# Performance work log

Hardware: AMD Instinct MI355X
Metric: run time of the kernel (lower is better)

Reference implementation:

```python
import jax, jax.numpy as jnp
import numpy as np

REFSIZE = 1024  # init kwarg refsize -> self.N
EPS = float(np.finfo(np.float32).eps)


def interp1d(x, y, xnew):
    """Batched linear interpolation, faithful to Interp1d.forward.
    x, y: (D, N) with x sorted along last dim; xnew: (D, P). Returns (D, P)."""
    # torch.searchsorted default (right=False) == numpy/jnp side='left'
    ind = jax.vmap(jnp.searchsorted)(x, xnew) - 1
    ind = jnp.clip(ind, 0, x.shape[1] - 2)
    slopes = (y[:, 1:] - y[:, :-1]) / (EPS + (x[:, 1:] - x[:, :-1]))
    x_sel = jnp.take_along_axis(x, ind, axis=1)
    y_sel = jnp.take_along_axis(y, ind, axis=1)
    s_sel = jnp.take_along_axis(slopes, ind, axis=1)
    return y_sel + s_sel * (xnew - x_sel)


def setup_inputs() -> dict:
    key = jax.random.key(0)
    k1, k2 = jax.random.split(key)
    l, n = 2048, 4096
    x1 = jax.random.uniform(k1, (l, n), dtype=jnp.float32)  # points on [0,1)
    w = jax.random.uniform(k2, (l, n), dtype=jnp.float32)
    x1_weights = w / jnp.sum(w, axis=-1, keepdims=True)  # row-normalized masses
    return {"x1": x1, "x1_weights": x1_weights}


def reference(x1, x1_weights):
    l, n = x1.shape
    N = REFSIZE
    ref = jnp.linspace(0.0, 1.0, N + 1, dtype=jnp.float32)[:-1]  # (N,)

    # empirical_cdf: sort samples, cumsum weights
    order = jnp.argsort(x1, axis=-1)
    xs = jnp.take_along_axis(x1, order, axis=-1)          # (l, n) sorted samples
    ys = jnp.cumsum(jnp.take_along_axis(x1_weights, order, axis=-1), axis=-1)  # CDF

    # emb
    alpha = (jnp.sum(x1 * x1_weights, axis=-1) / jnp.sum(x1_weights, axis=-1) - 0.5)[:, None]
    xnew = jnp.broadcast_to(jnp.linspace(-1.0, 2.0, 3 * N, dtype=jnp.float32)[None, :], (l, 3 * N))
    int_x = jnp.floor(xnew)
    rest_x = xnew - int_x
    ecdf = int_x + interp1d(xs, ys, rest_x)               # (l, 3N) extended CDF

    x_grid = jnp.broadcast_to(ref[None, :], (l, N))
    embedd = interp1d(ecdf, xnew, x_grid - alpha) - x_grid  # inverse-CDF embedding

    # circular cost
    a = jnp.abs(embedd)
    m = jnp.minimum(a, 1.0 - a)
    return jnp.sqrt(jnp.mean(jnp.sum(m * m, axis=-1)) + 1e-8)
```

## Files before the change

### kernel.cpp

```cpp
#include <hip/hip_runtime.h>
#include <math.h>

#define L    2048
#define NCOL 4096
#define NG   1024
#define N3   3072
#define T    256
#define EPT  16
#define NB   2048
#define BPT  (NB / T)
#define FEPS 1.1920929e-07f

typedef unsigned long long u64;

__device__ __forceinline__ int lower_bound_f(const float* a, int lo, int hi, float v) {
  while (lo < hi) {
    int mid = (lo + hi) >> 1;
    if (a[mid] < v) lo = mid + 1; else hi = mid;
  }
  return lo;
}

__device__ __forceinline__ int bucket_of(u64 k) {
  float f = __uint_as_float((unsigned)(k >> 32));
  int b = (int)(f * (float)NB);
  return b > NB - 1 ? NB - 1 : b;
}

__global__ __launch_bounds__(T, 3) void lcot_rows(const float* __restrict__ X,
                                                  const float* __restrict__ W,
                                                  float* __restrict__ rowsum) {
  extern __shared__ char smem[];
  u64*   pairs = (u64*)smem;
  float* xs    = (float*)smem;
  float* ys    = xs + NCOL;
  int*   cnt   = (int*)(smem + 32768);
  float* ecdf  = (float*)(smem + 32768 + 8200);

  __shared__ float redA[4], redB[4], fwt[4];
  __shared__ int   iwt[4];
  __shared__ float s_alpha;

  const int tid  = threadIdx.x;
  const int lane = tid & 63;
  const int wave = tid >> 6;
  const int row  = blockIdx.x;
  const float* xr = X + (size_t)row * NCOL;
  const float* wr = W + (size_t)row * NCOL;

#pragma unroll
  for (int i = 0; i < BPT; ++i) cnt[tid + i * T] = 0;

  u64 key[EPT]; float wv[EPT];
  float sxw = 0.f, sw = 0.f;
  const float4* xr4 = (const float4*)xr;
  const float4* wr4 = (const float4*)wr;
#pragma unroll
  for (int c = 0; c < 4; ++c) {
    float4 xv = xr4[tid * 4 + c];
    float4 ww = wr4[tid * 4 + c];
    sxw += xv.x * ww.x + xv.y * ww.y + xv.z * ww.z + xv.w * ww.w;
    sw  += ww.x + ww.y + ww.z + ww.w;
    int b = 16 * tid + 4 * c;
    key[4*c+0] = ((u64)__float_as_uint(xv.x) << 32) | (unsigned)(b + 0);
    key[4*c+1] = ((u64)__float_as_uint(xv.y) << 32) | (unsigned)(b + 1);
    key[4*c+2] = ((u64)__float_as_uint(xv.z) << 32) | (unsigned)(b + 2);
    key[4*c+3] = ((u64)__float_as_uint(xv.w) << 32) | (unsigned)(b + 3);
    wv[4*c+0] = ww.x; wv[4*c+1] = ww.y; wv[4*c+2] = ww.z; wv[4*c+3] = ww.w;
  }
#pragma unroll
  for (int off = 32; off > 0; off >>= 1) {
    sxw += __shfl_down(sxw, off);
    sw  += __shfl_down(sw, off);
  }
  if (lane == 0) { redA[wave] = sxw; redB[wave] = sw; }
  __syncthreads();

  int ord[EPT];
#pragma unroll
  for (int e = 0; e < EPT; ++e) ord[e] = atomicAdd(&cnt[bucket_of(key[e])], 1);
  __syncthreads();
  if (tid == 0)
    s_alpha = (redA[0] + redA[1] + redA[2] + redA[3]) /
              (redB[0] + redB[1] + redB[2] + redB[3]) - 0.5f;

  int c8[BPT];
  int runi = 0;
#pragma unroll
  for (int j = 0; j < BPT; ++j) { c8[j] = cnt[tid * BPT + j]; runi += c8[j]; }
  int toti = runi, prei = runi;
#pragma unroll
  for (int off = 1; off < 64; off <<= 1) {
    int v = __shfl_up(prei, off);
    if (lane >= off) prei += v;
  }
  if (lane == 63) iwt[wave] = prei;
  __syncthreads();
  int wpre = 0;
#pragma unroll
  for (int w2 = 0; w2 < 4; ++w2) wpre += (w2 < wave) ? iwt[w2] : 0;
  int acc = wpre + prei - toti;
#pragma unroll
  for (int j = 0; j < BPT; ++j) { int t2 = acc; acc += c8[j]; cnt[tid * BPT + j] = t2; }
  if (tid == T - 1) cnt[NB] = acc;
  __syncthreads();

#pragma unroll
  for (int e = 0; e < EPT; ++e) pairs[cnt[bucket_of(key[e])] + ord[e]] = key[e];
  __syncthreads();

  int p[EPT];
#pragma unroll
  for (int e = 0; e < EPT; ++e) {
    int b = bucket_of(key[e]);
    int lo = cnt[b], m = cnt[b + 1] - lo;
    int r = 0;
    for (int q = 0; q < m; ++q) r += (pairs[lo + q] < key[e]) ? 1 : 0;
    p[e] = lo + r;
  }
  __syncthreads();

#pragma unroll
  for (int e = 0; e < EPT; ++e) {
    xs[p[e]] = __uint_as_float((unsigned)(key[e] >> 32));
    ys[p[e]] = wv[e];
  }
  __syncthreads();

  float lw[EPT];
  {
    const float4* y4 = (const float4*)(ys + 16 * tid);
    float4 a0 = y4[0], a1 = y4[1], a2 = y4[2], a3 = y4[3];
    lw[0]=a0.x; lw[1]=a0.y; lw[2]=a0.z; lw[3]=a0.w;
    lw[4]=a1.x; lw[5]=a1.y; lw[6]=a1.z; lw[7]=a1.w;
    lw[8]=a2.x; lw[9]=a2.y; lw[10]=a2.z; lw[11]=a2.w;
    lw[12]=a3.x; lw[13]=a3.y; lw[14]=a3.z; lw[15]=a3.w;
  }
  float runf = 0.f;
#pragma unroll
  for (int c = 0; c < EPT; ++c) { runf += lw[c]; lw[c] = runf; }
  float totf = runf, pref = runf;
#pragma unroll
  for (int off = 1; off < 64; off <<= 1) {
    float v = __shfl_up(pref, off);
    if (lane >= off) pref += v;
  }
  if (lane == 63) fwt[wave] = pref;
  __syncthreads();
  float wpf = 0.f;
#pragma unroll
  for (int w2 = 0; w2 < 4; ++w2) wpf += (w2 < wave) ? fwt[w2] : 0.f;
  float basef = wpf + pref - totf;
  {
    float4* y4 = (float4*)(ys + 16 * tid);
    y4[0] = make_float4(basef+lw[0],  basef+lw[1],  basef+lw[2],  basef+lw[3]);
    y4[1] = make_float4(basef+lw[4],  basef+lw[5],  basef+lw[6],  basef+lw[7]);
    y4[2] = make_float4(basef+lw[8],  basef+lw[9],  basef+lw[10], basef+lw[11]);
    y4[3] = make_float4(basef+lw[12], basef+lw[13], basef+lw[14], basef+lw[15]);
  }
  __syncthreads();

#pragma unroll
  for (int s = 0; s < N3 / T; ++s) {
    int j = tid + s * T;
    float xnew = -1.0f + (3.0f * (float)j) / 3071.0f;
    float ix = floorf(xnew);
    float rest = xnew - ix;
    int k = (int)(rest * (float)NB);
    k = k > NB - 1 ? NB - 1 : k;
    int lo = lower_bound_f(xs, cnt[k], cnt[k + 1], rest);
    int ind = lo - 1;
    ind = ind < 0 ? 0 : (ind > NCOL - 2 ? NCOL - 2 : ind);
    float x0 = xs[ind], x1v = xs[ind + 1];
    float y0 = ys[ind], y1v = ys[ind + 1];
    float slope = (y1v - y0) / (FEPS + (x1v - x0));
    ecdf[j] = ix + (y0 + slope * (rest - x0));
  }
  __syncthreads();

  float alpha = s_alpha;
  float accf = 0.f;
#pragma unroll
  for (int s = 0; s < NG / T; ++s) {
    int kq = tid + s * T;
    float xg = (float)kq / 1024.0f;
    float q = xg - alpha;
    int lo = lower_bound_f(ecdf, 0, N3, q);
    int ind = lo - 1;
    ind = ind < 0 ? 0 : (ind > N3 - 2 ? N3 - 2 : ind);
    float e0 = ecdf[ind], e1 = ecdf[ind + 1];
    float y0 = -1.0f + (3.0f * (float)ind) / 3071.0f;
    float y1 = -1.0f + (3.0f * (float)(ind + 1)) / 3071.0f;
    float slope = (y1 - y0) / (FEPS + (e1 - e0));
    float emb = y0 + slope * (q - e0) - xg;
    float a = fabsf(emb);
    float m = fminf(a, 1.0f - a);
    accf += m * m;
  }
#pragma unroll
  for (int off = 32; off > 0; off >>= 1) accf += __shfl_down(accf, off);
  if (lane == 0) redA[wave] = accf;
  __syncthreads();
  if (tid == 0) rowsum[row] = redA[0] + redA[1] + redA[2] + redA[3];
}

__global__ __launch_bounds__(256) void lcot_final(const float* __restrict__ rowsum,
                                                  float* __restrict__ out) {
  __shared__ float red[4];
  int t = threadIdx.x;
  float s = 0.f;
  for (int i = t; i < L; i += 256) s += rowsum[i];
#pragma unroll
  for (int off = 32; off > 0; off >>= 1) s += __shfl_down(s, off);
  if ((t & 63) == 0) red[t >> 6] = s;
  __syncthreads();
  if (t == 0) {
    float tot = red[0] + red[1] + red[2] + red[3];
    out[0] = sqrtf(tot / (float)L + 1e-8f);
  }
}

extern "C" void kernel_launch(void* const* d_in, const int* in_sizes, int n_in,
                              void* d_out, int out_size, void* d_ws, size_t ws_size,
                              hipStream_t stream) {
  const float* X = (const float*)d_in[0];
  const float* W = (const float*)d_in[1];
  float* rowsum = (float*)d_ws;
  size_t shbytes = 32768 + 8200 + (size_t)N3 * 4;
  hipLaunchKernelGGL(lcot_rows, dim3(L), dim3(T), shbytes, stream, X, W, rowsum);
  hipLaunchKernelGGL(lcot_final, dim3(1), dim3(256), 0, stream,
                     (const float*)rowsum, (float*)d_out);
}
```

Baseline: 194.5 us.

## Double threads per row and add bucket LUT for inverse-CDF search

Raises the per-row block from 256 to 512 threads with 8 elements per thread, adjusting the scans and reductions for 8 waves. It also builds a 257-entry lookup table over the extended CDF so each inverse-CDF query binary-searches a narrow window instead of all 3072 entries. The aim is more latency hiding per row and fewer LDS probes in the second search. The cost is more LDS per block and an extra barrier. The windowed search assumes the CDF maps each bucket to a small index range.

```diff
diff --git a/kernel.cpp b/kernel.cpp
--- a/kernel.cpp
+++ b/kernel.cpp
@@ -5,8 +5,9 @@
 #define NCOL 4096
 #define NG   1024
 #define N3   3072
-#define T    256
-#define EPT  16
+#define T    512
+#define NW   8
+#define EPT  8
 #define NB   2048
 #define BPT  (NB / T)
 #define FEPS 1.1920929e-07f
@@ -27,7 +28,7 @@
   return b > NB - 1 ? NB - 1 : b;
 }
 
-__global__ __launch_bounds__(T, 3) void lcot_rows(const float* __restrict__ X,
+__global__ __launch_bounds__(T, 2) void lcot_rows(const float* __restrict__ X,
                                                   const float* __restrict__ W,
                                                   float* __restrict__ rowsum) {
   extern __shared__ char smem[];
@@ -35,10 +36,11 @@
   float* xs    = (float*)smem;
   float* ys    = xs + NCOL;
   int*   cnt   = (int*)(smem + 32768);
-  float* ecdf  = (float*)(smem + 32768 + 8200);
-
-  __shared__ float redA[4], redB[4], fwt[4];
-  __shared__ int   iwt[4];
+  float* ecdf  = (float*)(smem + 32768 + 8208);
+  unsigned short* lut2 = (unsigned short*)(smem + 32768 + 8208 + 12288);
+
+  __shared__ float redA[NW], redB[NW], fwt[NW];
+  __shared__ int   iwt[NW];
   __shared__ float s_alpha;
 
   const int tid  = threadIdx.x;
@@ -56,12 +58,12 @@
   const float4* xr4 = (const float4*)xr;
   const float4* wr4 = (const float4*)wr;
 #pragma unroll
-  for (int c = 0; c < 4; ++c) {
-    float4 xv = xr4[tid * 4 + c];
-    float4 ww = wr4[tid * 4 + c];
+  for (int c = 0; c < 2; ++c) {
+    float4 xv = xr4[tid * 2 + c];
+    float4 ww = wr4[tid * 2 + c];
     sxw += xv.x * ww.x + xv.y * ww.y + xv.z * ww.z + xv.w * ww.w;
     sw  += ww.x + ww.y + ww.z + ww.w;
-    int b = 16 * tid + 4 * c;
+    int b = 8 * tid + 4 * c;
     key[4*c+0] = ((u64)__float_as_uint(xv.x) << 32) | (unsigned)(b + 0);
     key[4*c+1] = ((u64)__float_as_uint(xv.y) << 32) | (unsigned)(b + 1);
     key[4*c+2] = ((u64)__float_as_uint(xv.z) << 32) | (unsigned)(b + 2);
@@ -80,14 +82,17 @@
 #pragma unroll
   for (int e = 0; e < EPT; ++e) ord[e] = atomicAdd(&cnt[bucket_of(key[e])], 1);
   __syncthreads();
-  if (tid == 0)
-    s_alpha = (redA[0] + redA[1] + redA[2] + redA[3]) /
-              (redB[0] + redB[1] + redB[2] + redB[3]) - 0.5f;
-
-  int c8[BPT];
+  if (tid == 0) {
+    float a = 0.f, b = 0.f;
+#pragma unroll
+    for (int i = 0; i < NW; ++i) { a += redA[i]; b += redB[i]; }
+    s_alpha = a / b - 0.5f;
+  }
+
+  int c4[BPT];
   int runi = 0;
 #pragma unroll
-  for (int j = 0; j < BPT; ++j) { c8[j] = cnt[tid * BPT + j]; runi += c8[j]; }
+  for (int j = 0; j < BPT; ++j) { c4[j] = cnt[tid * BPT + j]; runi += c4[j]; }
   int toti = runi, prei = runi;
 #pragma unroll
   for (int off = 1; off < 64; off <<= 1) {
@@ -98,10 +103,10 @@
   __syncthreads();
   int wpre = 0;
 #pragma unroll
-  for (int w2 = 0; w2 < 4; ++w2) wpre += (w2 < wave) ? iwt[w2] : 0;
+  for (int w2 = 0; w2 < NW; ++w2) wpre += (w2 < wave) ? iwt[w2] : 0;
   int acc = wpre + prei - toti;
 #pragma unroll
-  for (int j = 0; j < BPT; ++j) { int t2 = acc; acc += c8[j]; cnt[tid * BPT + j] = t2; }
+  for (int j = 0; j < BPT; ++j) { int t2 = acc; acc += c4[j]; cnt[tid * BPT + j] = t2; }
   if (tid == T - 1) cnt[NB] = acc;
   __syncthreads();
 
@@ -129,12 +134,10 @@
 
   float lw[EPT];
   {
-    const float4* y4 = (const float4*)(ys + 16 * tid);
-    float4 a0 = y4[0], a1 = y4[1], a2 = y4[2], a3 = y4[3];
+    const float4* y4 = (const float4*)(ys + EPT * tid);
+    float4 a0 = y4[0], a1 = y4[1];
     lw[0]=a0.x; lw[1]=a0.y; lw[2]=a0.z; lw[3]=a0.w;
     lw[4]=a1.x; lw[5]=a1.y; lw[6]=a1.z; lw[7]=a1.w;
-    lw[8]=a2.x; lw[9]=a2.y; lw[10]=a2.z; lw[11]=a2.w;
-    lw[12]=a3.x; lw[13]=a3.y; lw[14]=a3.z; lw[15]=a3.w;
   }
   float runf = 0.f;
 #pragma unroll
@@ -149,14 +152,12 @@
   __syncthreads();
   float wpf = 0.f;
 #pragma unroll
-  for (int w2 = 0; w2 < 4; ++w2) wpf += (w2 < wave) ? fwt[w2] : 0.f;
+  for (int w2 = 0; w2 < NW; ++w2) wpf += (w2 < wave) ? fwt[w2] : 0.f;
   float basef = wpf + pref - totf;
   {
-    float4* y4 = (float4*)(ys + 16 * tid);
-    y4[0] = make_float4(basef+lw[0],  basef+lw[1],  basef+lw[2],  basef+lw[3]);
-    y4[1] = make_float4(basef+lw[4],  basef+lw[5],  basef+lw[6],  basef+lw[7]);
-    y4[2] = make_float4(basef+lw[8],  basef+lw[9],  basef+lw[10], basef+lw[11]);
-    y4[3] = make_float4(basef+lw[12], basef+lw[13], basef+lw[14], basef+lw[15]);
+    float4* y4 = (float4*)(ys + EPT * tid);
+    y4[0] = make_float4(basef+lw[0], basef+lw[1], basef+lw[2], basef+lw[3]);
+    y4[1] = make_float4(basef+lw[4], basef+lw[5], basef+lw[6], basef+lw[7]);
   }
   __syncthreads();
 
@@ -178,6 +179,12 @@
   }
   __syncthreads();
 
+  if (tid < 257) {
+    float v = -1.0f + 3.0f * (float)tid * (1.0f / 256.0f);
+    lut2[tid] = (unsigned short)lower_bound_f(ecdf, 0, N3, v);
+  }
+  __syncthreads();
+
   float alpha = s_alpha;
   float accf = 0.f;
 #pragma unroll
@@ -185,7 +192,11 @@
     int kq = tid + s * T;
     float xg = (float)kq / 1024.0f;
     float q = xg - alpha;
-    int lo = lower_bound_f(ecdf, 0, N3, q);
+    int k2 = (int)floorf((q + 1.0f) * (256.0f / 3.0f));
+    k2 = k2 < 0 ? 0 : (k2 > 255 ? 255 : k2);
+    int blo = k2 > 0 ? k2 - 1 : 0;
+    int bhi = k2 < 254 ? k2 + 2 : 256;
+    int lo = lower_bound_f(ecdf, lut2[blo], lut2[bhi], q);
     int ind = lo - 1;
     ind = ind < 0 ? 0 : (ind > N3 - 2 ? N3 - 2 : ind);
     float e0 = ecdf[ind], e1 = ecdf[ind + 1];
@@ -201,7 +212,12 @@
   for (int off = 32; off > 0; off >>= 1) accf += __shfl_down(accf, off);
   if (lane == 0) redA[wave] = accf;
   __syncthreads();
-  if (tid == 0) rowsum[row] = redA[0] + redA[1] + redA[2] + redA[3];
+  if (tid == 0) {
+    float s = 0.f;
+#pragma unroll
+    for (int i = 0; i < NW; ++i) s += redA[i];
+    rowsum[row] = s;
+  }
 }
 
 __global__ __launch_bounds__(256) void lcot_final(const float* __restrict__ rowsum,
@@ -226,7 +242,7 @@
   const float* X = (const float*)d_in[0];
   const float* W = (const float*)d_in[1];
   float* rowsum = (float*)d_ws;
-  size_t shbytes = 32768 + 8200 + (size_t)N3 * 4;
+  size_t shbytes = 32768 + 8208 + 12288 + 520;
   hipLaunchKernelGGL(lcot_rows, dim3(L), dim3(T), shbytes, stream, X, W, rowsum);
   hipLaunchKernelGGL(lcot_final, dim3(1), dim3(256), 0, stream,
                      (const float*)rowsum, (float*)d_out);
```

New measurement: 189.7 us. 1.03x faster.
